# Optimization experiments

Hardware: AMD Instinct MI355X
Metric: run time of the kernel (lower is better)

Reference implementation:

```python
import jax, jax.numpy as jnp
import numpy as np

BN_EPS = 1e-5
TAU = 1.0  # gumbel temperature

def setup_inputs() -> dict:
    key = jax.random.key(0)
    ks = jax.random.split(key, 6)
    B, O, F, H, HID = 32, 4096, 256, 8, 128
    x = jax.random.normal(ks[0], (B, O, F), dtype=jnp.float32)
    gumbel_noise = jax.random.gumbel(ks[1], (B, O, H), dtype=jnp.float32)
    W_in = jax.random.normal(ks[2], (F, HID), dtype=jnp.float32) * (1.0 / np.sqrt(F))
    b_in = jnp.zeros((HID,), jnp.float32)
    W_blk = jax.random.normal(ks[3], (HID, HID), dtype=jnp.float32) * (1.0 / np.sqrt(HID))
    b_blk = jnp.zeros((HID,), jnp.float32)
    bn_gamma = jnp.ones((HID,), jnp.float32)
    bn_beta = jnp.zeros((HID,), jnp.float32)
    W_fc = jax.random.normal(ks[4], (HID, H), dtype=jnp.float32) * (1.0 / np.sqrt(HID))
    b_fc = jnp.zeros((H,), jnp.float32)
    return {"x": x, "gumbel_noise": gumbel_noise, "W_in": W_in, "b_in": b_in,
            "W_blk": W_blk, "b_blk": b_blk, "bn_gamma": bn_gamma, "bn_beta": bn_beta,
            "W_fc": W_fc, "b_fc": b_fc}

def reference(x, gumbel_noise, W_in, b_in, W_blk, b_blk, bn_gamma, bn_beta, W_fc, b_fc):
    B, O, F = x.shape
    xf = x.reshape(B * O, F)
    # DynamicNetwork head: input linear + relu, one residual block (Linear+BN+ReLU), fc
    h = jax.nn.relu(xf @ W_in + b_in)  # (B*O, HID)
    z = h @ W_blk + b_blk
    mu = z.mean(axis=0)
    var = z.var(axis=0)  # biased var, matches BatchNorm training normalization
    z = (z - mu) * jax.lax.rsqrt(var + BN_EPS) * bn_gamma + bn_beta
    h = jax.nn.relu(z) + h  # residual
    logits = (h @ W_fc + b_fc).reshape(B, O, -1)  # (B, O, H)
    # mask out zero-norm observations
    mask = (jnp.linalg.norm(x, axis=2) != 0)[..., None].astype(x.dtype)  # (B, O, 1)
    logits = logits * mask
    # gumbel softmax over observation dim (soft)
    w = jax.nn.softmax((logits + gumbel_noise) / TAU, axis=1)  # (B, O, H)
    # weighted sum pooling: algebraically the repeat-multiply-sum in the original
    pooled = jnp.einsum('boh,bof->bhf', w, x)  # (B, H, F)
    return pooled.reshape(B, -1)  # (B, H*F)
```

## Files before the change

### kernel.cpp

```cpp
#include <hip/hip_runtime.h>
#include <hip/hip_bf16.h>
#include <math.h>

#define MB_ 131072
#define F_  256
#define HID_ 128
#define H_  8
#define O_  4096
#define B_  32

typedef __attribute__((ext_vector_type(8))) short short8;
typedef __attribute__((ext_vector_type(4))) float f32x4;

static __device__ __forceinline__ unsigned short f2bf(float f) {
    unsigned int u = __float_as_uint(f);
    unsigned int r = (u + 0x7fffu + ((u >> 16) & 1u)) >> 16;
    return (unsigned short)r;
}
static __device__ __forceinline__ float bf2f(unsigned short u) {
    return __uint_as_float(((unsigned int)u) << 16);
}
static __device__ __forceinline__ float bflo(unsigned int u) {
    return __uint_as_float(u << 16);
}
static __device__ __forceinline__ float bfhi(unsigned int u) {
    return __uint_as_float(u & 0xffff0000u);
}

__global__ __launch_bounds__(256) void k_prep(
    const float* __restrict__ W_in, const float* __restrict__ W_blk,
    unsigned short* __restrict__ WinT, unsigned short* __restrict__ WblkT)
{
    const int idx = blockIdx.x * 256 + threadIdx.x;
    if (idx < 32768) {
        const int n = idx >> 8, k = idx & 255;
        WinT[idx] = f2bf(W_in[(size_t)k * HID_ + n]);
    } else {
        const int i2 = idx - 32768;
        const int n = i2 >> 7, k = i2 & 127;
        WblkT[i2] = f2bf(W_blk[(size_t)k * HID_ + n]);
    }
}

__global__ __launch_bounds__(256) void k_mfma_in(
    const float* __restrict__ x, const unsigned short* __restrict__ WinT,
    const float* __restrict__ b_in,
    unsigned short* __restrict__ h_out, float* __restrict__ mask_out)
{
    __shared__ unsigned short a_s[128 * 40];
    __shared__ unsigned short b_s[128 * 40];
    __shared__ float msum_s[128];
    const int tid = threadIdx.x;
    const int R0 = blockIdx.x * 128;
    const int lp_r = tid >> 3;
    const int lp_c = tid & 7;
    const int wave = tid >> 6;
    const int wrow = wave >> 1, wcol = wave & 1;
    const int lane = tid & 63;
    const int lm = lane & 15, quad = lane >> 4;

    if (tid < 128) msum_s[tid] = 0.f;
    float ms[4] = {0.f, 0.f, 0.f, 0.f};

    f32x4 acc[4][4];
#pragma unroll
    for (int i = 0; i < 4; i++)
#pragma unroll
        for (int j = 0; j < 4; j++) acc[i][j] = (f32x4){0.f, 0.f, 0.f, 0.f};

    for (int kt = 0; kt < 8; kt++) {
#pragma unroll
        for (int p = 0; p < 4; p++) {
            const int r = lp_r + 32 * p;
            const float4 v = *(const float4*)(x + (size_t)(R0 + r) * F_ + kt * 32 + lp_c * 4);
            ms[p] += v.x * v.x + v.y * v.y + v.z * v.z + v.w * v.w;
            ushort4 o;
            o.x = f2bf(v.x); o.y = f2bf(v.y); o.z = f2bf(v.z); o.w = f2bf(v.w);
            *(ushort4*)(&a_s[r * 40 + lp_c * 4]) = o;
        }
#pragma unroll
        for (int p = 0; p < 4; p++) {
            const int n = lp_r + 32 * p;
            const ushort4 wv = *(const ushort4*)(WinT + (size_t)n * F_ + kt * 32 + lp_c * 4);
            *(ushort4*)(&b_s[n * 40 + lp_c * 4]) = wv;
        }
        __syncthreads();
        short8 af[4], bfr[4];
#pragma unroll
        for (int mi = 0; mi < 4; mi++)
            af[mi] = *(const short8*)(&a_s[(wrow * 64 + mi * 16 + lm) * 40 + quad * 8]);
#pragma unroll
        for (int ni = 0; ni < 4; ni++)
            bfr[ni] = *(const short8*)(&b_s[(wcol * 64 + ni * 16 + lm) * 40 + quad * 8]);
#pragma unroll
        for (int mi = 0; mi < 4; mi++)
#pragma unroll
            for (int ni = 0; ni < 4; ni++)
                acc[mi][ni] = __builtin_amdgcn_mfma_f32_16x16x32_bf16(af[mi], bfr[ni], acc[mi][ni], 0, 0, 0);
        __syncthreads();
    }

#pragma unroll
    for (int p = 0; p < 4; p++) atomicAdd(&msum_s[lp_r + 32 * p], ms[p]);

    float bcol[4];
#pragma unroll
    for (int ni = 0; ni < 4; ni++) bcol[ni] = b_in[wcol * 64 + ni * 16 + lm];
#pragma unroll
    for (int mi = 0; mi < 4; mi++)
#pragma unroll
        for (int r = 0; r < 4; r++) {
            const size_t row = (size_t)R0 + wrow * 64 + mi * 16 + quad * 4 + r;
#pragma unroll
            for (int ni = 0; ni < 4; ni++) {
                const float v = fmaxf(acc[mi][ni][r] + bcol[ni], 0.f);
                h_out[row * HID_ + wcol * 64 + ni * 16 + lm] = f2bf(v);
            }
        }
    __syncthreads();
    if (tid < 128) mask_out[R0 + tid] = (msum_s[tid] != 0.f) ? 1.f : 0.f;
}

__global__ __launch_bounds__(256) void k_mfma_blk(
    const unsigned short* __restrict__ h_in, const unsigned short* __restrict__ WblkT,
    const float* __restrict__ b_blk, unsigned short* __restrict__ z_out,
    float* __restrict__ sumP, float* __restrict__ sumsqP)
{
    __shared__ unsigned short a_s[128 * 40];
    __shared__ unsigned short b_s[128 * 40];
    __shared__ float csum_s[128], csumsq_s[128];
    const int tid = threadIdx.x;
    const int R0 = blockIdx.x * 128;
    const int lp_r = tid >> 3;
    const int lp_c = tid & 7;
    const int wave = tid >> 6;
    const int wrow = wave >> 1, wcol = wave & 1;
    const int lane = tid & 63;
    const int lm = lane & 15, quad = lane >> 4;

    if (tid < 128) { csum_s[tid] = 0.f; csumsq_s[tid] = 0.f; }

    f32x4 acc[4][4];
#pragma unroll
    for (int i = 0; i < 4; i++)
#pragma unroll
        for (int j = 0; j < 4; j++) acc[i][j] = (f32x4){0.f, 0.f, 0.f, 0.f};

    for (int kt = 0; kt < 4; kt++) {
#pragma unroll
        for (int p = 0; p < 4; p++) {
            const int r = lp_r + 32 * p;
            const ushort4 v = *(const ushort4*)(h_in + (size_t)(R0 + r) * HID_ + kt * 32 + lp_c * 4);
            *(ushort4*)(&a_s[r * 40 + lp_c * 4]) = v;
        }
#pragma unroll
        for (int p = 0; p < 4; p++) {
            const int n = lp_r + 32 * p;
            const ushort4 wv = *(const ushort4*)(WblkT + (size_t)n * HID_ + kt * 32 + lp_c * 4);
            *(ushort4*)(&b_s[n * 40 + lp_c * 4]) = wv;
        }
        __syncthreads();
        short8 af[4], bfr[4];
#pragma unroll
        for (int mi = 0; mi < 4; mi++)
            af[mi] = *(const short8*)(&a_s[(wrow * 64 + mi * 16 + lm) * 40 + quad * 8]);
#pragma unroll
        for (int ni = 0; ni < 4; ni++)
            bfr[ni] = *(const short8*)(&b_s[(wcol * 64 + ni * 16 + lm) * 40 + quad * 8]);
#pragma unroll
        for (int mi = 0; mi < 4; mi++)
#pragma unroll
            for (int ni = 0; ni < 4; ni++)
                acc[mi][ni] = __builtin_amdgcn_mfma_f32_16x16x32_bf16(af[mi], bfr[ni], acc[mi][ni], 0, 0, 0);
        __syncthreads();
    }

    float bcol[4];
#pragma unroll
    for (int ni = 0; ni < 4; ni++) bcol[ni] = b_blk[wcol * 64 + ni * 16 + lm];
    float s_c[4] = {0.f, 0.f, 0.f, 0.f}, ss_c[4] = {0.f, 0.f, 0.f, 0.f};
#pragma unroll
    for (int mi = 0; mi < 4; mi++)
#pragma unroll
        for (int r = 0; r < 4; r++) {
            const size_t row = (size_t)R0 + wrow * 64 + mi * 16 + quad * 4 + r;
#pragma unroll
            for (int ni = 0; ni < 4; ni++) {
                const float zv = acc[mi][ni][r] + bcol[ni];
                s_c[ni] += zv;
                ss_c[ni] += zv * zv;
                z_out[row * HID_ + wcol * 64 + ni * 16 + lm] = f2bf(zv);
            }
        }
#pragma unroll
    for (int ni = 0; ni < 4; ni++) {
        atomicAdd(&csum_s[wcol * 64 + ni * 16 + lm], s_c[ni]);
        atomicAdd(&csumsq_s[wcol * 64 + ni * 16 + lm], ss_c[ni]);
    }
    __syncthreads();
    if (tid < 128) {
        sumP[(size_t)blockIdx.x * 128 + tid] = csum_s[tid];
        sumsqP[(size_t)blockIdx.x * 128 + tid] = csumsq_s[tid];
    }
}

__global__ __launch_bounds__(256) void k_bnfin(
    const float* __restrict__ sumP, const float* __restrict__ sumsqP,
    const float* __restrict__ gamma, const float* __restrict__ beta,
    float* __restrict__ scale, float* __restrict__ shift)
{
    const int c = blockIdx.x;
    const int tid = threadIdx.x;
    float s = 0.f, ss = 0.f;
    for (int i = tid; i < 1024; i += 256) {
        s  += sumP[(size_t)i * 128 + c];
        ss += sumsqP[(size_t)i * 128 + c];
    }
#pragma unroll
    for (int off = 32; off; off >>= 1) {
        s  += __shfl_xor(s, off, 64);
        ss += __shfl_xor(ss, off, 64);
    }
    __shared__ float rs[4], rss[4];
    const int wid = tid >> 6, lane = tid & 63;
    if (lane == 0) { rs[wid] = s; rss[wid] = ss; }
    __syncthreads();
    if (tid == 0) {
        const float S  = rs[0] + rs[1] + rs[2] + rs[3];
        const float SS = rss[0] + rss[1] + rss[2] + rss[3];
        const float inv_m = 1.0f / (float)MB_;
        const float mu = S * inv_m;
        const float var = SS * inv_m - mu * mu;
        const float sc = gamma[c] * rsqrtf(var + 1e-5f);
        scale[c] = sc;
        shift[c] = beta[c] - mu * sc;
    }
}

__global__ __launch_bounds__(256) void k_logits(
    const unsigned short* __restrict__ h_in, const unsigned short* __restrict__ z_in,
    const float* __restrict__ scale, const float* __restrict__ shift,
    const float* __restrict__ W_fc, const float* __restrict__ b_fc,
    const float* __restrict__ mask, const float* __restrict__ gumbel,
    float* __restrict__ t_out)
{
    __shared__ float wfc_s[128 * 8];
    __shared__ float sc_s[128], sh_s[128];
    const int tid = threadIdx.x;
    for (int i = tid; i < 1024; i += 256) wfc_s[i] = W_fc[i];
    if (tid < 128) { sc_s[tid] = scale[tid]; sh_s[tid] = shift[tid]; }
    __syncthreads();

    const size_t row = (size_t)blockIdx.x * 256 + tid;
    float acc[8];
#pragma unroll
    for (int j = 0; j < 8; j++) acc[j] = 0.f;

    const uint4* hp = (const uint4*)(h_in + row * HID_);
    const uint4* zp = (const uint4*)(z_in + row * HID_);
#pragma unroll 2
    for (int kc = 0; kc < 16; kc++) {
        const uint4 hq = hp[kc];
        const uint4 zq = zp[kc];
        unsigned int hs[4] = {hq.x, hq.y, hq.z, hq.w};
        unsigned int zs[4] = {zq.x, zq.y, zq.z, zq.w};
#pragma unroll
        for (int p = 0; p < 4; p++) {
            const int k = kc * 8 + p * 2;
            const float hf0 = bflo(hs[p]), hf1 = bfhi(hs[p]);
            const float zf0 = bflo(zs[p]), zf1 = bfhi(zs[p]);
            const float hb0 = fmaxf(zf0 * sc_s[k] + sh_s[k], 0.f) + hf0;
            const float hb1 = fmaxf(zf1 * sc_s[k + 1] + sh_s[k + 1], 0.f) + hf1;
#pragma unroll
            for (int j = 0; j < 8; j++)
                acc[j] += hb0 * wfc_s[k * 8 + j] + hb1 * wfc_s[(k + 1) * 8 + j];
        }
    }
    const float mk = mask[row];
    const float4 g0 = *(const float4*)(gumbel + row * 8);
    const float4 g1 = *(const float4*)(gumbel + row * 8 + 4);
    float4 t0, t1;
    t0.x = (acc[0] + b_fc[0]) * mk + g0.x;
    t0.y = (acc[1] + b_fc[1]) * mk + g0.y;
    t0.z = (acc[2] + b_fc[2]) * mk + g0.z;
    t0.w = (acc[3] + b_fc[3]) * mk + g0.w;
    t1.x = (acc[4] + b_fc[4]) * mk + g1.x;
    t1.y = (acc[5] + b_fc[5]) * mk + g1.y;
    t1.z = (acc[6] + b_fc[6]) * mk + g1.z;
    t1.w = (acc[7] + b_fc[7]) * mk + g1.w;
    *(float4*)(t_out + row * 8) = t0;
    *(float4*)(t_out + row * 8 + 4) = t1;
}

__global__ __launch_bounds__(256) void k_softmax(
    const float* __restrict__ t_in, float* __restrict__ w_out)
{
    const int bh = blockIdx.x;
    const int b = bh >> 3, hh = bh & 7;
    const int tid = threadIdx.x;
    const float* tp = t_in + (size_t)b * O_ * H_ + hh;
    float v[16];
    float mx = -3.4e38f;
#pragma unroll
    for (int it = 0; it < 16; it++) {
        v[it] = tp[(size_t)(it * 256 + tid) * 8];
        mx = fmaxf(mx, v[it]);
    }
#pragma unroll
    for (int off = 32; off; off >>= 1) mx = fmaxf(mx, __shfl_xor(mx, off, 64));
    __shared__ float rm[4];
    __shared__ float rsum[4];
    const int wid = tid >> 6, lane = tid & 63;
    if (lane == 0) rm[wid] = mx;
    __syncthreads();
    mx = fmaxf(fmaxf(rm[0], rm[1]), fmaxf(rm[2], rm[3]));
    float sum = 0.f;
#pragma unroll
    for (int it = 0; it < 16; it++) { v[it] = __expf(v[it] - mx); sum += v[it]; }
#pragma unroll
    for (int off = 32; off; off >>= 1) sum += __shfl_xor(sum, off, 64);
    if (lane == 0) rsum[wid] = sum;
    __syncthreads();
    sum = rsum[0] + rsum[1] + rsum[2] + rsum[3];
    const float inv = 1.f / sum;
    float* wp = w_out + (size_t)bh * O_;
#pragma unroll
    for (int it = 0; it < 16; it++) wp[it * 256 + tid] = v[it] * inv;
}

__global__ __launch_bounds__(256) void k_pool(
    const float* __restrict__ x, const float* __restrict__ w_in,
    float* __restrict__ pp)
{
    __shared__ float ws_s[8][256];
    const int tid = threadIdx.x;
    const int oc = blockIdx.x;
    const int b = blockIdx.y;
#pragma unroll
    for (int hh = 0; hh < 8; hh++)
        ws_s[hh][tid] = w_in[((size_t)(b * 8 + hh)) * O_ + oc * 256 + tid];
    __syncthreads();
    float acc[8];
#pragma unroll
    for (int hh = 0; hh < 8; hh++) acc[hh] = 0.f;
    const float* xp = x + ((size_t)b * O_ + oc * 256) * F_ + tid;
    for (int o = 0; o < 256; o++) {
        const float xv = xp[(size_t)o * F_];
#pragma unroll
        for (int hh = 0; hh < 8; hh++) acc[hh] += ws_s[hh][o] * xv;
    }
    float* outp = pp + ((size_t)oc * 32 + b) * 2048;
#pragma unroll
    for (int hh = 0; hh < 8; hh++) outp[hh * 256 + tid] = acc[hh];
}

__global__ __launch_bounds__(256) void k_reduce_pool(
    const float* __restrict__ pp, float* __restrict__ out)
{
    const size_t i = (size_t)blockIdx.x * 256 + threadIdx.x;
    float s = 0.f;
#pragma unroll
    for (int oc = 0; oc < 16; oc++) s += pp[(size_t)oc * 65536 + i];
    out[i] = s;
}

extern "C" void kernel_launch(void* const* d_in, const int* in_sizes, int n_in,
                              void* d_out, int out_size, void* d_ws, size_t ws_size,
                              hipStream_t stream)
{
    const float* x      = (const float*)d_in[0];
    const float* gumbel = (const float*)d_in[1];
    const float* W_in   = (const float*)d_in[2];
    const float* b_in   = (const float*)d_in[3];
    const float* W_blk  = (const float*)d_in[4];
    const float* b_blk  = (const float*)d_in[5];
    const float* gamma  = (const float*)d_in[6];
    const float* beta   = (const float*)d_in[7];
    const float* W_fc   = (const float*)d_in[8];
    const float* b_fc   = (const float*)d_in[9];
    float* out = (float*)d_out;
    char* ws = (char*)d_ws;

    unsigned short* h_bf  = (unsigned short*)(ws + 0);
    unsigned short* z_bf  = (unsigned short*)(ws + 33554432);
    float* mask   = (float*)(ws + 67108864);
    float* sumP   = (float*)(ws + 67633152);
    float* sumsqP = (float*)(ws + 68157440);
    float* scale  = (float*)(ws + 68681728);
    float* shift  = (float*)(ws + 68682240);
    float* t_buf  = (float*)(ws + 68682752);
    float* w_buf  = (float*)(ws + 72877056);
    float* pp     = (float*)(ws + 77071360);
    unsigned short* WinT  = (unsigned short*)(ws + 81265664);
    unsigned short* WblkT = (unsigned short*)(ws + 81331200);

    k_prep<<<192, 256, 0, stream>>>(W_in, W_blk, WinT, WblkT);
    k_mfma_in<<<1024, 256, 0, stream>>>(x, WinT, b_in, h_bf, mask);
    k_mfma_blk<<<1024, 256, 0, stream>>>(h_bf, WblkT, b_blk, z_bf, sumP, sumsqP);
    k_bnfin<<<128, 256, 0, stream>>>(sumP, sumsqP, gamma, beta, scale, shift);
    k_logits<<<512, 256, 0, stream>>>(h_bf, z_bf, scale, shift, W_fc, b_fc, mask, gumbel, t_buf);
    k_softmax<<<256, 256, 0, stream>>>(t_buf, w_buf);
    k_pool<<<dim3(16, 32), 256, 0, stream>>>(x, w_buf, pp);
    k_reduce_pool<<<256, 256, 0, stream>>>(pp, out);
}
```

Baseline: 303.7 us.

## Fuse both GEMMs, fold softmax into logits max and pooling normalization

The input and block GEMMs now run in one kernel: the relu'd h tile stays in shared memory and feeds the second MFMA pass, so h no longer has to be re-read from global memory. The separate softmax kernel is removed. Logits compute a per-batch per-head max with ordered-key atomicMax, and pooling applies exp on the fly, writing partial sums and denominators. Pooling uses more, smaller blocks, and the final reduce divides by the total. Risks include pp aliasing the h buffer (which is only safe because h is dead by then) and extra atomics.

```diff
diff --git a/kernel.cpp b/kernel.cpp
--- a/kernel.cpp
+++ b/kernel.cpp
@@ -1,5 +1,4 @@
 #include <hip/hip_runtime.h>
-#include <hip/hip_bf16.h>
 #include <math.h>
 
 #define MB_ 131072
@@ -17,21 +16,24 @@
     unsigned int r = (u + 0x7fffu + ((u >> 16) & 1u)) >> 16;
     return (unsigned short)r;
 }
-static __device__ __forceinline__ float bf2f(unsigned short u) {
-    return __uint_as_float(((unsigned int)u) << 16);
-}
 static __device__ __forceinline__ float bflo(unsigned int u) {
     return __uint_as_float(u << 16);
 }
 static __device__ __forceinline__ float bfhi(unsigned int u) {
     return __uint_as_float(u & 0xffff0000u);
 }
+static __device__ __forceinline__ unsigned int fkey(float f) {
+    unsigned int u = __float_as_uint(f);
+    return (u & 0x80000000u) ? ~u : (u | 0x80000000u);
+}
 
 __global__ __launch_bounds__(256) void k_prep(
     const float* __restrict__ W_in, const float* __restrict__ W_blk,
-    unsigned short* __restrict__ WinT, unsigned short* __restrict__ WblkT)
+    unsigned short* __restrict__ WinT, unsigned short* __restrict__ WblkT,
+    unsigned int* __restrict__ Mmax)
 {
     const int idx = blockIdx.x * 256 + threadIdx.x;
+    if (idx < 256) Mmax[idx] = 0u;
     if (idx < 32768) {
         const int n = idx >> 8, k = idx & 255;
         WinT[idx] = f2bf(W_in[(size_t)k * HID_ + n]);
@@ -42,14 +44,20 @@
     }
 }
 
-__global__ __launch_bounds__(256) void k_mfma_in(
+__global__ __launch_bounds__(256) void k_fused(
     const float* __restrict__ x, const unsigned short* __restrict__ WinT,
     const float* __restrict__ b_in,
-    unsigned short* __restrict__ h_out, float* __restrict__ mask_out)
-{
-    __shared__ unsigned short a_s[128 * 40];
-    __shared__ unsigned short b_s[128 * 40];
+    const unsigned short* __restrict__ WblkT, const float* __restrict__ b_blk,
+    unsigned short* __restrict__ h_out, unsigned short* __restrict__ z_out,
+    float* __restrict__ mask_out,
+    float* __restrict__ sumP, float* __restrict__ sumsqP)
+{
+    __shared__ unsigned short smem[128 * 136];
     __shared__ float msum_s[128];
+    __shared__ float csum_s[128], csumsq_s[128];
+    unsigned short* a_s = smem;
+    unsigned short* b_s = smem + 5120;
+
     const int tid = threadIdx.x;
     const int R0 = blockIdx.x * 128;
     const int lp_r = tid >> 3;
@@ -59,7 +67,7 @@
     const int lane = tid & 63;
     const int lm = lane & 15, quad = lane >> 4;
 
-    if (tid < 128) msum_s[tid] = 0.f;
+    if (tid < 128) { msum_s[tid] = 0.f; csum_s[tid] = 0.f; csumsq_s[tid] = 0.f; }
     float ms[4] = {0.f, 0.f, 0.f, 0.f};
 
     f32x4 acc[4][4];
@@ -103,9 +111,54 @@
 #pragma unroll
     for (int p = 0; p < 4; p++) atomicAdd(&msum_s[lp_r + 32 * p], ms[p]);
 
-    float bcol[4];
-#pragma unroll
-    for (int ni = 0; ni < 4; ni++) bcol[ni] = b_in[wcol * 64 + ni * 16 + lm];
+    {
+        float bcol[4];
+#pragma unroll
+        for (int ni = 0; ni < 4; ni++) bcol[ni] = b_in[wcol * 64 + ni * 16 + lm];
+#pragma unroll
+        for (int mi = 0; mi < 4; mi++)
+#pragma unroll
+            for (int r = 0; r < 4; r++) {
+                const int rl = wrow * 64 + mi * 16 + quad * 4 + r;
+                const size_t grow = (size_t)(R0 + rl) * HID_;
+#pragma unroll
+                for (int ni = 0; ni < 4; ni++) {
+                    const int col = wcol * 64 + ni * 16 + lm;
+                    const float v = fmaxf(acc[mi][ni][r] + bcol[ni], 0.f);
+                    const unsigned short us = f2bf(v);
+                    h_out[grow + col] = us;
+                    smem[rl * 136 + col] = us;
+                }
+            }
+    }
+#pragma unroll
+    for (int i = 0; i < 4; i++)
+#pragma unroll
+        for (int j = 0; j < 4; j++) acc[i][j] = (f32x4){0.f, 0.f, 0.f, 0.f};
+    __syncthreads();
+
+    if (tid < 128) mask_out[R0 + tid] = (msum_s[tid] != 0.f) ? 1.f : 0.f;
+
+#pragma unroll
+    for (int kt = 0; kt < 4; kt++) {
+        short8 af[4], bfr[4];
+#pragma unroll
+        for (int mi = 0; mi < 4; mi++)
+            af[mi] = *(const short8*)(&smem[(wrow * 64 + mi * 16 + lm) * 136 + kt * 32 + quad * 8]);
+#pragma unroll
+        for (int ni = 0; ni < 4; ni++)
+            bfr[ni] = *(const short8*)(WblkT + (size_t)(wcol * 64 + ni * 16 + lm) * HID_ + kt * 32 + quad * 8);
+#pragma unroll
+        for (int mi = 0; mi < 4; mi++)
+#pragma unroll
+            for (int ni = 0; ni < 4; ni++)
+                acc[mi][ni] = __builtin_amdgcn_mfma_f32_16x16x32_bf16(af[mi], bfr[ni], acc[mi][ni], 0, 0, 0);
+    }
+
+    float bcol2[4];
+#pragma unroll
+    for (int ni = 0; ni < 4; ni++) bcol2[ni] = b_blk[wcol * 64 + ni * 16 + lm];
+    float s_c[4] = {0.f, 0.f, 0.f, 0.f}, ss_c[4] = {0.f, 0.f, 0.f, 0.f};
 #pragma unroll
     for (int mi = 0; mi < 4; mi++)
 #pragma unroll
@@ -113,80 +166,7 @@
             const size_t row = (size_t)R0 + wrow * 64 + mi * 16 + quad * 4 + r;
 #pragma unroll
             for (int ni = 0; ni < 4; ni++) {
-                const float v = fmaxf(acc[mi][ni][r] + bcol[ni], 0.f);
-                h_out[row * HID_ + wcol * 64 + ni * 16 + lm] = f2bf(v);
-            }
-        }
-    __syncthreads();
-    if (tid < 128) mask_out[R0 + tid] = (msum_s[tid] != 0.f) ? 1.f : 0.f;
-}
-
-__global__ __launch_bounds__(256) void k_mfma_blk(
-    const unsigned short* __restrict__ h_in, const unsigned short* __restrict__ WblkT,
-    const float* __restrict__ b_blk, unsigned short* __restrict__ z_out,
-    float* __restrict__ sumP, float* __restrict__ sumsqP)
-{
-    __shared__ unsigned short a_s[128 * 40];
-    __shared__ unsigned short b_s[128 * 40];
-    __shared__ float csum_s[128], csumsq_s[128];
-    const int tid = threadIdx.x;
-    const int R0 = blockIdx.x * 128;
-    const int lp_r = tid >> 3;
-    const int lp_c = tid & 7;
-    const int wave = tid >> 6;
-    const int wrow = wave >> 1, wcol = wave & 1;
-    const int lane = tid & 63;
-    const int lm = lane & 15, quad = lane >> 4;
-
-    if (tid < 128) { csum_s[tid] = 0.f; csumsq_s[tid] = 0.f; }
-
-    f32x4 acc[4][4];
-#pragma unroll
-    for (int i = 0; i < 4; i++)
-#pragma unroll
-        for (int j = 0; j < 4; j++) acc[i][j] = (f32x4){0.f, 0.f, 0.f, 0.f};
-
-    for (int kt = 0; kt < 4; kt++) {
-#pragma unroll
-        for (int p = 0; p < 4; p++) {
-            const int r = lp_r + 32 * p;
-            const ushort4 v = *(const ushort4*)(h_in + (size_t)(R0 + r) * HID_ + kt * 32 + lp_c * 4);
-            *(ushort4*)(&a_s[r * 40 + lp_c * 4]) = v;
-        }
-#pragma unroll
-        for (int p = 0; p < 4; p++) {
-            const int n = lp_r + 32 * p;
-            const ushort4 wv = *(const ushort4*)(WblkT + (size_t)n * HID_ + kt * 32 + lp_c * 4);
-            *(ushort4*)(&b_s[n * 40 + lp_c * 4]) = wv;
-        }
-        __syncthreads();
-        short8 af[4], bfr[4];
-#pragma unroll
-        for (int mi = 0; mi < 4; mi++)
-            af[mi] = *(const short8*)(&a_s[(wrow * 64 + mi * 16 + lm) * 40 + quad * 8]);
-#pragma unroll
-        for (int ni = 0; ni < 4; ni++)
-            bfr[ni] = *(const short8*)(&b_s[(wcol * 64 + ni * 16 + lm) * 40 + quad * 8]);
-#pragma unroll
-        for (int mi = 0; mi < 4; mi++)
-#pragma unroll
-            for (int ni = 0; ni < 4; ni++)
-                acc[mi][ni] = __builtin_amdgcn_mfma_f32_16x16x32_bf16(af[mi], bfr[ni], acc[mi][ni], 0, 0, 0);
-        __syncthreads();
-    }
-
-    float bcol[4];
-#pragma unroll
-    for (int ni = 0; ni < 4; ni++) bcol[ni] = b_blk[wcol * 64 + ni * 16 + lm];
-    float s_c[4] = {0.f, 0.f, 0.f, 0.f}, ss_c[4] = {0.f, 0.f, 0.f, 0.f};
-#pragma unroll
-    for (int mi = 0; mi < 4; mi++)
-#pragma unroll
-        for (int r = 0; r < 4; r++) {
-            const size_t row = (size_t)R0 + wrow * 64 + mi * 16 + quad * 4 + r;
-#pragma unroll
-            for (int ni = 0; ni < 4; ni++) {
-                const float zv = acc[mi][ni][r] + bcol[ni];
+                const float zv = acc[mi][ni][r] + bcol2[ni];
                 s_c[ni] += zv;
                 ss_c[ni] += zv * zv;
                 z_out[row * HID_ + wcol * 64 + ni * 16 + lm] = f2bf(zv);
@@ -242,109 +222,134 @@
     const float* __restrict__ scale, const float* __restrict__ shift,
     const float* __restrict__ W_fc, const float* __restrict__ b_fc,
     const float* __restrict__ mask, const float* __restrict__ gumbel,
-    float* __restrict__ t_out)
-{
-    __shared__ float wfc_s[128 * 8];
+    float* __restrict__ t_out, unsigned int* __restrict__ Mmax)
+{
+    __shared__ float wfc_s[1024];
     __shared__ float sc_s[128], sh_s[128];
     const int tid = threadIdx.x;
     for (int i = tid; i < 1024; i += 256) wfc_s[i] = W_fc[i];
     if (tid < 128) { sc_s[tid] = scale[tid]; sh_s[tid] = shift[tid]; }
     __syncthreads();
 
-    const size_t row = (size_t)blockIdx.x * 256 + tid;
-    float acc[8];
-#pragma unroll
-    for (int j = 0; j < 8; j++) acc[j] = 0.f;
-
-    const uint4* hp = (const uint4*)(h_in + row * HID_);
-    const uint4* zp = (const uint4*)(z_in + row * HID_);
+    const size_t row0 = (size_t)blockIdx.x * 512 + tid;
+    const size_t row1 = row0 + 256;
+    float a0[8], a1[8];
+#pragma unroll
+    for (int j = 0; j < 8; j++) { a0[j] = 0.f; a1[j] = 0.f; }
+
+    const uint4* hp0 = (const uint4*)(h_in + row0 * HID_);
+    const uint4* zq0 = (const uint4*)(z_in + row0 * HID_);
+    const uint4* hp1 = (const uint4*)(h_in + row1 * HID_);
+    const uint4* zq1 = (const uint4*)(z_in + row1 * HID_);
+
 #pragma unroll 2
     for (int kc = 0; kc < 16; kc++) {
-        const uint4 hq = hp[kc];
-        const uint4 zq = zp[kc];
-        unsigned int hs[4] = {hq.x, hq.y, hq.z, hq.w};
-        unsigned int zs[4] = {zq.x, zq.y, zq.z, zq.w};
+        const uint4 h0 = hp0[kc], z0 = zq0[kc];
+        const uint4 h1 = hp1[kc], z1 = zq1[kc];
+        const unsigned int hs0[4] = {h0.x, h0.y, h0.z, h0.w};
+        const unsigned int zs0[4] = {z0.x, z0.y, z0.z, z0.w};
+        const unsigned int hs1[4] = {h1.x, h1.y, h1.z, h1.w};
+        const unsigned int zs1[4] = {z1.x, z1.y, z1.z, z1.w};
 #pragma unroll
         for (int p = 0; p < 4; p++) {
             const int k = kc * 8 + p * 2;
-            const float hf0 = bflo(hs[p]), hf1 = bfhi(hs[p]);
-            const float zf0 = bflo(zs[p]), zf1 = bfhi(zs[p]);
-            const float hb0 = fmaxf(zf0 * sc_s[k] + sh_s[k], 0.f) + hf0;
-            const float hb1 = fmaxf(zf1 * sc_s[k + 1] + sh_s[k + 1], 0.f) + hf1;
-#pragma unroll
-            for (int j = 0; j < 8; j++)
-                acc[j] += hb0 * wfc_s[k * 8 + j] + hb1 * wfc_s[(k + 1) * 8 + j];
+            const float sck0 = sc_s[k], shk0 = sh_s[k];
+            const float sck1 = sc_s[k + 1], shk1 = sh_s[k + 1];
+            const float4 wA = *(const float4*)&wfc_s[k * 8];
+            const float4 wB = *(const float4*)&wfc_s[k * 8 + 4];
+            const float4 wC = *(const float4*)&wfc_s[k * 8 + 8];
+            const float4 wD = *(const float4*)&wfc_s[k * 8 + 12];
+            {
+                const float hf0 = bflo(hs0[p]), hf1 = bfhi(hs0[p]);
+                const float zf0 = bflo(zs0[p]), zf1 = bfhi(zs0[p]);
+                const float hb0 = fmaxf(zf0 * sck0 + shk0, 0.f) + hf0;
+                const float hb1 = fmaxf(zf1 * sck1 + shk1, 0.f) + hf1;
+                a0[0] += hb0 * wA.x + hb1 * wC.x;  a0[1] += hb0 * wA.y + hb1 * wC.y;
+                a0[2] += hb0 * wA.z + hb1 * wC.z;  a0[3] += hb0 * wA.w + hb1 * wC.w;
+                a0[4] += hb0 * wB.x + hb1 * wD.x;  a0[5] += hb0 * wB.y + hb1 * wD.y;
+                a0[6] += hb0 * wB.z + hb1 * wD.z;  a0[7] += hb0 * wB.w + hb1 * wD.w;
+            }
+            {
+                const float hf0 = bflo(hs1[p]), hf1 = bfhi(hs1[p]);
+                const float zf0 = bflo(zs1[p]), zf1 = bfhi(zs1[p]);
+                const float hb0 = fmaxf(zf0 * sck0 + shk0, 0.f) + hf0;
+                const float hb1 = fmaxf(zf1 * sck1 + shk1, 0.f) + hf1;
+                a1[0] += hb0 * wA.x + hb1 * wC.x;  a1[1] += hb0 * wA.y + hb1 * wC.y;
+                a1[2] += hb0 * wA.z + hb1 * wC.z;  a1[3] += hb0 * wA.w + hb1 * wC.w;
+                a1[4] += hb0 * wB.x + hb1 * wD.x;  a1[5] += hb0 * wB.y + hb1 * wD.y;
+                a1[6] += hb0 * wB.z + hb1 * wD.z;  a1[7] += hb0 * wB.w + hb1 * wD.w;
+            }
         }
     }
-    const float mk = mask[row];
-    const float4 g0 = *(const float4*)(gumbel + row * 8);
-    const float4 g1 = *(const float4*)(gumbel + row * 8 + 4);
-    float4 t0, t1;
-    t0.x = (acc[0] + b_fc[0]) * mk + g0.x;
-    t0.y = (acc[1] + b_fc[1]) * mk + g0.y;
-    t0.z = (acc[2] + b_fc[2]) * mk + g0.z;
-    t0.w = (acc[3] + b_fc[3]) * mk + g0.w;
-    t1.x = (acc[4] + b_fc[4]) * mk + g1.x;
-    t1.y = (acc[5] + b_fc[5]) * mk + g1.y;
-    t1.z = (acc[6] + b_fc[6]) * mk + g1.z;
-    t1.w = (acc[7] + b_fc[7]) * mk + g1.w;
-    *(float4*)(t_out + row * 8) = t0;
-    *(float4*)(t_out + row * 8 + 4) = t1;
-}
-
-__global__ __launch_bounds__(256) void k_softmax(
-    const float* __restrict__ t_in, float* __restrict__ w_out)
-{
-    const int bh = blockIdx.x;
-    const int b = bh >> 3, hh = bh & 7;
-    const int tid = threadIdx.x;
-    const float* tp = t_in + (size_t)b * O_ * H_ + hh;
-    float v[16];
-    float mx = -3.4e38f;
-#pragma unroll
-    for (int it = 0; it < 16; it++) {
-        v[it] = tp[(size_t)(it * 256 + tid) * 8];
-        mx = fmaxf(mx, v[it]);
-    }
-#pragma unroll
-    for (int off = 32; off; off >>= 1) mx = fmaxf(mx, __shfl_xor(mx, off, 64));
-    __shared__ float rm[4];
-    __shared__ float rsum[4];
-    const int wid = tid >> 6, lane = tid & 63;
-    if (lane == 0) rm[wid] = mx;
-    __syncthreads();
-    mx = fmaxf(fmaxf(rm[0], rm[1]), fmaxf(rm[2], rm[3]));
-    float sum = 0.f;
-#pragma unroll
-    for (int it = 0; it < 16; it++) { v[it] = __expf(v[it] - mx); sum += v[it]; }
-#pragma unroll
-    for (int off = 32; off; off >>= 1) sum += __shfl_xor(sum, off, 64);
-    if (lane == 0) rsum[wid] = sum;
-    __syncthreads();
-    sum = rsum[0] + rsum[1] + rsum[2] + rsum[3];
-    const float inv = 1.f / sum;
-    float* wp = w_out + (size_t)bh * O_;
-#pragma unroll
-    for (int it = 0; it < 16; it++) wp[it * 256 + tid] = v[it] * inv;
+
+    float bf[8];
+#pragma unroll
+    for (int j = 0; j < 8; j++) bf[j] = b_fc[j];
+    const float mk0 = mask[row0], mk1 = mask[row1];
+    float g0[8], g1[8];
+    *(float4*)&g0[0] = *(const float4*)(gumbel + row0 * 8);
+    *(float4*)&g0[4] = *(const float4*)(gumbel + row0 * 8 + 4);
+    *(float4*)&g1[0] = *(const float4*)(gumbel + row1 * 8);
+    *(float4*)&g1[4] = *(const float4*)(gumbel + row1 * 8 + 4);
+    float t0[8], t1[8];
+#pragma unroll
+    for (int j = 0; j < 8; j++) {
+        t0[j] = (a0[j] + bf[j]) * mk0 + g0[j];
+        t1[j] = (a1[j] + bf[j]) * mk1 + g1[j];
+    }
+    *(float4*)(t_out + row0 * 8)     = *(float4*)&t0[0];
+    *(float4*)(t_out + row0 * 8 + 4) = *(float4*)&t0[4];
+    *(float4*)(t_out + row1 * 8)     = *(float4*)&t1[0];
+    *(float4*)(t_out + row1 * 8 + 4) = *(float4*)&t1[4];
+
+    float tm[8];
+#pragma unroll
+    for (int j = 0; j < 8; j++) tm[j] = fmaxf(t0[j], t1[j]);
+#pragma unroll
+    for (int off = 32; off; off >>= 1)
+#pragma unroll
+        for (int j = 0; j < 8; j++) tm[j] = fmaxf(tm[j], __shfl_xor(tm[j], off, 64));
+    if ((tid & 63) == 0) {
+        const int bb = blockIdx.x >> 3;
+#pragma unroll
+        for (int j = 0; j < 8; j++) atomicMax(&Mmax[bb * 8 + j], fkey(tm[j]));
+    }
 }
 
 __global__ __launch_bounds__(256) void k_pool(
-    const float* __restrict__ x, const float* __restrict__ w_in,
-    float* __restrict__ pp)
-{
-    __shared__ float ws_s[8][256];
+    const float* __restrict__ x, const float* __restrict__ t_in,
+    const unsigned int* __restrict__ Mmax,
+    float* __restrict__ pp, float* __restrict__ zp)
+{
+    __shared__ float ws_s[8][64];
+    __shared__ float M_s[8];
     const int tid = threadIdx.x;
     const int oc = blockIdx.x;
-    const int b = blockIdx.y;
-#pragma unroll
-    for (int hh = 0; hh < 8; hh++)
-        ws_s[hh][tid] = w_in[((size_t)(b * 8 + hh)) * O_ + oc * 256 + tid];
-    __syncthreads();
+    const int b  = blockIdx.y;
+    if (tid < 8) {
+        const unsigned int k = Mmax[b * 8 + tid];
+        const unsigned int s = (k & 0x80000000u) ? (k & 0x7fffffffu) : ~k;
+        M_s[tid] = __uint_as_float(s);
+    }
+    __syncthreads();
+#pragma unroll
+    for (int i = tid; i < 512; i += 256) {
+        const int ol = i >> 3, hh = i & 7;
+        const float tv = t_in[((size_t)b * O_ + oc * 64 + ol) * H_ + hh];
+        ws_s[hh][ol] = __expf(tv - M_s[hh]);
+    }
+    __syncthreads();
+    if (tid < 8) {
+        float s = 0.f;
+        for (int o = 0; o < 64; o++) s += ws_s[tid][o];
+        zp[((size_t)oc * 32 + b) * 8 + tid] = s;
+    }
     float acc[8];
 #pragma unroll
     for (int hh = 0; hh < 8; hh++) acc[hh] = 0.f;
-    const float* xp = x + ((size_t)b * O_ + oc * 256) * F_ + tid;
-    for (int o = 0; o < 256; o++) {
+    const float* xp = x + ((size_t)b * O_ + oc * 64) * F_ + tid;
+#pragma unroll 4
+    for (int o = 0; o < 64; o++) {
         const float xv = xp[(size_t)o * F_];
 #pragma unroll
         for (int hh = 0; hh < 8; hh++) acc[hh] += ws_s[hh][o] * xv;
@@ -354,14 +359,26 @@
     for (int hh = 0; hh < 8; hh++) outp[hh * 256 + tid] = acc[hh];
 }
 
-__global__ __launch_bounds__(256) void k_reduce_pool(
-    const float* __restrict__ pp, float* __restrict__ out)
-{
-    const size_t i = (size_t)blockIdx.x * 256 + threadIdx.x;
+__global__ __launch_bounds__(256) void k_reduce(
+    const float* __restrict__ pp, const float* __restrict__ zp,
+    float* __restrict__ out)
+{
+    const int blk = blockIdx.x;
+    const int b = blk >> 3, hh = blk & 7;
+    const int tid = threadIdx.x;
+    __shared__ float invZ_s;
+    if (tid < 64) {
+        float z = zp[((size_t)tid * 32 + b) * 8 + hh];
+#pragma unroll
+        for (int off = 32; off; off >>= 1) z += __shfl_xor(z, off, 64);
+        if (tid == 0) invZ_s = 1.f / z;
+    }
+    __syncthreads();
     float s = 0.f;
-#pragma unroll
-    for (int oc = 0; oc < 16; oc++) s += pp[(size_t)oc * 65536 + i];
-    out[i] = s;
+    const float* p0 = pp + (size_t)b * 2048 + hh * 256 + tid;
+#pragma unroll 8
+    for (int ocq = 0; ocq < 64; ocq++) s += p0[(size_t)ocq * 65536];
+    out[(size_t)b * 2048 + hh * 256 + tid] = s * invZ_s;
 }
 
 extern "C" void kernel_launch(void* const* d_in, const int* in_sizes, int n_in,
@@ -382,6 +399,8 @@
     char* ws = (char*)d_ws;
 
     unsigned short* h_bf  = (unsigned short*)(ws + 0);
+    float* pp     = (float*)(ws + 0);
+    float* zp     = (float*)(ws + 16777216);
     unsigned short* z_bf  = (unsigned short*)(ws + 33554432);
     float* mask   = (float*)(ws + 67108864);
     float* sumP   = (float*)(ws + 67633152);
@@ -389,17 +408,14 @@
     float* scale  = (float*)(ws + 68681728);
     float* shift  = (float*)(ws + 68682240);
     float* t_buf  = (float*)(ws + 68682752);
-    float* w_buf  = (float*)(ws + 72877056);
-    float* pp     = (float*)(ws + 77071360);
-    unsigned short* WinT  = (unsigned short*)(ws + 81265664);
-    unsigned short* WblkT = (unsigned short*)(ws + 81331200);
-
-    k_prep<<<192, 256, 0, stream>>>(W_in, W_blk, WinT, WblkT);
-    k_mfma_in<<<1024, 256, 0, stream>>>(x, WinT, b_in, h_bf, mask);
-    k_mfma_blk<<<1024, 256, 0, stream>>>(h_bf, WblkT, b_blk, z_bf, sumP, sumsqP);
+    unsigned int* Mmax = (unsigned int*)(ws + 72877056);
+    unsigned short* WinT  = (unsigned short*)(ws + 72878080);
+    unsigned short* WblkT = (unsigned short*)(ws + 72943616);
+
+    k_prep<<<192, 256, 0, stream>>>(W_in, W_blk, WinT, WblkT, Mmax);
+    k_fused<<<1024, 256, 0, stream>>>(x, WinT, b_in, WblkT, b_blk, h_bf, z_bf, mask, sumP, sumsqP);
     k_bnfin<<<128, 256, 0, stream>>>(sumP, sumsqP, gamma, beta, scale, shift);
-    k_logits<<<512, 256, 0, stream>>>(h_bf, z_bf, scale, shift, W_fc, b_fc, mask, gumbel, t_buf);
-    k_softmax<<<256, 256, 0, stream>>>(t_buf, w_buf);
-    k_pool<<<dim3(16, 32), 256, 0, stream>>>(x, w_buf, pp);
-    k_reduce_pool<<<256, 256, 0, stream>>>(pp, out);
-}
+    k_logits<<<256, 256, 0, stream>>>(h_bf, z_bf, scale, shift, W_fc, b_fc, mask, gumbel, t_buf, Mmax);
+    k_pool<<<dim3(64, 32), 256, 0, stream>>>(x, t_buf, Mmax, pp, zp);
+    k_reduce<<<256, 256, 0, stream>>>(pp, zp, out);
+}
```

Measured after the change: 304.9 us. No clear change (+0.4%).
